# Performance work log

Hardware: AMD Instinct MI355X
Metric: run time of the kernel (lower is better)

Reference implementation:

```python
import jax, jax.numpy as jnp
import numpy as np
from jax import lax

B, N, T, F_IN = 16, 500, 256, 8
H, K, OUT = 64, 3, 1
EPS = 1e-5


def setup_inputs() -> dict:
    key = jax.random.key(0)
    ks = jax.random.split(key, 20)
    def xavier(k, shape):
        fan_in, fan_out = shape[-2], shape[-1]
        lim = np.sqrt(6.0 / (fan_in + fan_out))
        return jax.random.uniform(k, shape, jnp.float32, -lim, lim)
    inp = {
        'x': jax.random.normal(ks[0], (B, N, T, F_IN), jnp.float32),
        'adj': jax.random.uniform(ks[1], (N, N), jnp.float32),
        # temporal conv layer 1: in=F_IN, layer 2: in=H; kernel (1,K), OIHW
        'conv_w1': jax.random.normal(ks[2], (H, F_IN, 1, K), jnp.float32) * 0.1,
        'conv_b1': jnp.zeros((H,), jnp.float32),
        'conv_w2': jax.random.normal(ks[3], (H, H, 1, K), jnp.float32) * 0.05,
        'conv_b2': jnp.zeros((H,), jnp.float32),
        # graph conv weights (in,out) + bias
        'gcn_w1': xavier(ks[4], (H, H)),
        'gcn_b1': jnp.zeros((H,), jnp.float32),
        'gcn_w2': xavier(ks[5], (H, H)),
        'gcn_b2': jnp.zeros((H,), jnp.float32),
        # batchnorm (eval mode: running stats)
        'bn_g1': jnp.ones((H,), jnp.float32),
        'bn_be1': jnp.zeros((H,), jnp.float32),
        'bn_m1': jax.random.normal(ks[6], (H,), jnp.float32) * 0.1,
        'bn_v1': jnp.ones((H,), jnp.float32),
        'bn_g2': jnp.ones((H,), jnp.float32),
        'bn_be2': jnp.zeros((H,), jnp.float32),
        'bn_m2': jax.random.normal(ks[7], (H,), jnp.float32) * 0.1,
        'bn_v2': jnp.ones((H,), jnp.float32),
        # output MLP H -> H//2 -> OUT
        'out_w1': xavier(ks[8], (H, H // 2)),
        'out_bb1': jnp.zeros((H // 2,), jnp.float32),
        'out_w2': xavier(ks[9], (H // 2, OUT)),
        'out_bb2': jnp.zeros((OUT,), jnp.float32),
    }
    return inp


def _layer(x, adj, cw, cb, gw, gb, bg, bb, bm, bv):
    # x: (B, C_in, N, T)
    x = lax.conv_general_dilated(
        x, cw, window_strides=(1, 1), padding=[(0, 0), (K // 2, K // 2)],
        dimension_numbers=('NCHW', 'OIHW', 'NCHW'))
    x = jax.nn.relu(x + cb[None, :, None, None])           # (B,H,N,T)
    # batched graph conv over all timesteps at once
    s = jnp.einsum('bcnt,ch->bhnt', x, gw)                 # support = x @ W
    x = jnp.einsum('mn,bhnt->bhmt', adj, s) + gb[None, :, None, None]
    x = jax.nn.relu(x)
    # batchnorm2d eval over channel dim
    x = (x - bm[None, :, None, None]) * (bg / jnp.sqrt(bv + EPS))[None, :, None, None] + bb[None, :, None, None]
    return x  # dropout is identity in eval


def reference(x, adj, conv_w1, conv_b1, conv_w2, conv_b2,
              gcn_w1, gcn_b1, gcn_w2, gcn_b2,
              bn_g1, bn_be1, bn_m1, bn_v1,
              bn_g2, bn_be2, bn_m2, bn_v2,
              out_w1, out_bb1, out_w2, out_bb2):
    h = jnp.transpose(x, (0, 3, 1, 2))                      # (B,F_in,N,T)
    h = _layer(h, adj, conv_w1, conv_b1, gcn_w1, gcn_b1, bn_g1, bn_be1, bn_m1, bn_v1)
    h = _layer(h, adj, conv_w2, conv_b2, gcn_w2, gcn_b2, bn_g2, bn_be2, bn_m2, bn_v2)
    h = h.mean(axis=-1)                                     # (B,H,N)
    h = jnp.transpose(h, (0, 2, 1))                         # (B,N,H)
    h = jax.nn.relu(h @ out_w1 + out_bb1)
    return h @ out_w2 + out_bb2                             # (B,N,OUT)
```

## Files before the change

### kernel.cpp

```cpp
#include <hip/hip_runtime.h>
#include <hip/hip_bf16.h>


#define BB 16
#define NN 500
#define TT 256
#define FIN 8
#define HH 64

using bf16 = __hip_bfloat16;
typedef __attribute__((ext_vector_type(8))) short short8;
typedef __attribute__((ext_vector_type(4))) short short4v;
typedef __attribute__((ext_vector_type(4))) float f32x4;

static __device__ __forceinline__ short bf16bits(float v) {
    __hip_bfloat16 h = __float2bfloat16(v);
    return *reinterpret_cast<short*>(&h);
}

__global__ __launch_bounds__(256) void k_prep_adj(
    const float* __restrict__ adj, bf16* __restrict__ adjb)
{
    int i = blockIdx.x * 256 + threadIdx.x;
    if (i < 512 * 512) {
        int r = i >> 9, c = i & 511;
        float v = (r < NN && c < NN) ? adj[r * NN + c] : 0.f;
        adjb[i] = __float2bfloat16(v);
    }
}

__global__ __launch_bounds__(256) void k_prep_weights(
    const float* __restrict__ cw1, const float* __restrict__ gw1,
    const float* __restrict__ w2,  const float* __restrict__ gw2,
    bf16* __restrict__ wA1, bf16* __restrict__ gA1,
    bf16* __restrict__ wA2, bf16* __restrict__ gA2)
{
    int i = blockIdx.x * 256 + threadIdx.x;
    if (i < 2048) {
        int h = i >> 5, kp = i & 31, kk = kp >> 3, f = kp & 7;
        wA1[i] = __float2bfloat16(kk < 3 ? cw1[(h * 8 + f) * 3 + kk] : 0.f);
    } else if (i < 6144) {
        int j = i - 2048, h = j >> 6, c = j & 63;
        gA1[j] = __float2bfloat16(gw1[c * 64 + h]);
    } else if (i < 18432) {
        int j = i - 6144, kk = j / 4096, r = j & 4095, co = r >> 6, ci = r & 63;
        wA2[j] = __float2bfloat16(w2[(co * 64 + ci) * 3 + kk]);
    } else if (i < 22528) {
        int j = i - 18432, h = j >> 6, c = j & 63;
        gA2[j] = __float2bfloat16(gw2[c * 64 + h]);
    }
}

__global__ __launch_bounds__(256) void k_conv_mfma1(
    const float* __restrict__ x, const bf16* __restrict__ wA1,
    const bf16* __restrict__ gA1, const float* __restrict__ cb,
    bf16* __restrict__ s_out)
{
    __shared__ __align__(16) short xs[256 * 64];

    const int tid = threadIdx.x;
    const int n = blockIdx.x, lb = blockIdx.y;
    const int lane = tid & 63, w = tid >> 6;
    const int lr = lane & 15, kg = lane >> 4;
    const int t0w = w * 64;

    {
        const float4* gx = (const float4*)(x + (size_t)(lb * NN + n) * (TT * FIN) + tid * 8);
        float4 a = gx[0], b = gx[1];
        short8 v;
        v[0] = bf16bits(a.x); v[1] = bf16bits(a.y); v[2] = bf16bits(a.z); v[3] = bf16bits(a.w);
        v[4] = bf16bits(b.x); v[5] = bf16bits(b.y); v[6] = bf16bits(b.z); v[7] = bf16bits(b.w);
        const int t = tid;
        *(short8*)((char*)xs + t * 128 + (16 ^ ((t & 7) << 4))) = v;
        if (t < 255)
            *(short8*)((char*)xs + (t + 1) * 128 + (0 ^ (((t + 1) & 7) << 4))) = v;
        if (t > 0)
            *(short8*)((char*)xs + (t - 1) * 128 + (32 ^ (((t - 1) & 7) << 4))) = v;
        short8 z = {0, 0, 0, 0, 0, 0, 0, 0};
        *(short8*)((char*)xs + t * 128 + (48 ^ ((t & 7) << 4))) = z;
        if (t == 0)   *(short8*)((char*)xs + 0 * 128 + (0 ^ 0)) = z;
        if (t == 255) *(short8*)((char*)xs + 255 * 128 + (32 ^ ((255 & 7) << 4))) = z;
    }
    __syncthreads();

    f32x4 acc[4][4];
    #pragma unroll
    for (int mi = 0; mi < 4; mi++)
        #pragma unroll
        for (int ti = 0; ti < 4; ti++)
            acc[mi][ti] = (f32x4){0.f, 0.f, 0.f, 0.f};

    const short* wAp = (const short*)wA1;
    {
        short8 af[4], bfr[4];
        #pragma unroll
        for (int mi = 0; mi < 4; mi++)
            af[mi] = *(const short8*)(wAp + (mi * 16 + lr) * 32 + kg * 8);
        #pragma unroll
        for (int ti = 0; ti < 4; ti++) {
            const int row = t0w + ti * 16 + lr;
            bfr[ti] = *(const short8*)((const char*)xs + row * 128 + ((kg * 16) ^ ((row & 7) << 4)));
        }
        #pragma unroll
        for (int ti = 0; ti < 4; ti++)
            #pragma unroll
            for (int mi = 0; mi < 4; mi++)
                acc[mi][ti] = __builtin_amdgcn_mfma_f32_16x16x32_bf16(af[mi], bfr[ti], acc[mi][ti], 0, 0, 0);
    }
    __syncthreads();

    {
        float cbl[16];
        #pragma unroll
        for (int mi = 0; mi < 4; mi++)
            #pragma unroll
            for (int r = 0; r < 4; r++) cbl[mi * 4 + r] = cb[mi * 16 + kg * 4 + r];
        #pragma unroll
        for (int mi = 0; mi < 4; mi++) {
            #pragma unroll
            for (int ti = 0; ti < 4; ti++) {
                const int t = t0w + ti * 16 + lr;
                short4v yv;
                #pragma unroll
                for (int r = 0; r < 4; r++)
                    yv[r] = bf16bits(fmaxf(acc[mi][ti][r] + cbl[mi * 4 + r], 0.f));
                *(short4v*)((char*)xs + t * 128 + ((mi * 32 + kg * 8) ^ ((t & 7) << 4))) = yv;
            }
        }
    }
    __syncthreads();

    f32x4 acc2[4][4];
    #pragma unroll
    for (int mi = 0; mi < 4; mi++)
        #pragma unroll
        for (int ti = 0; ti < 4; ti++)
            acc2[mi][ti] = (f32x4){0.f, 0.f, 0.f, 0.f};

    const short* gAp = (const short*)gA1;
    #pragma unroll
    for (int ks = 0; ks < 2; ks++) {
        short8 af[4], bfr[4];
        #pragma unroll
        for (int mi = 0; mi < 4; mi++)
            af[mi] = *(const short8*)(gAp + (mi * 16 + lr) * 64 + ks * 32 + kg * 8);
        #pragma unroll
        for (int ti = 0; ti < 4; ti++) {
            const int t = t0w + ti * 16 + lr;
            bfr[ti] = *(const short8*)((const char*)xs + t * 128 + ((ks * 64 + kg * 16) ^ ((t & 7) << 4)));
        }
        #pragma unroll
        for (int ti = 0; ti < 4; ti++)
            #pragma unroll
            for (int mi = 0; mi < 4; mi++)
                acc2[mi][ti] = __builtin_amdgcn_mfma_f32_16x16x32_bf16(af[mi], bfr[ti], acc2[mi][ti], 0, 0, 0);
    }

    #pragma unroll
    for (int mi = 0; mi < 4; mi++) {
        #pragma unroll
        for (int r = 0; r < 4; r++) {
            const int h = mi * 16 + kg * 4 + r;
            bf16* orow = s_out + ((size_t)(lb * 64 + h) * NN + n) * TT + t0w + lr;
            #pragma unroll
            for (int ti = 0; ti < 4; ti++)
                orow[ti * 16] = __float2bfloat16(acc2[mi][ti][r]);
        }
    }
}

#define SWZ_T(t) (((((t) & 7) ^ (((t) >> 5) << 1)) & 7) << 4)

template<bool MEAN>
__global__ __launch_bounds__(256) void k_adj_mfma(
    const bf16* __restrict__ s_in, const bf16* __restrict__ adjb,
    const float* __restrict__ gb, const float* __restrict__ bn_g,
    const float* __restrict__ bn_b, const float* __restrict__ bn_m,
    const float* __restrict__ bn_v, bf16* __restrict__ h_out,
    float* __restrict__ pf)
{
    __shared__ __align__(16) short AsS[128 * 72];
    __shared__ __align__(16) short BtS[128 * 64];

    const int tid = threadIdx.x;
    const int m0 = (blockIdx.x >> 1) * 128;
    const int t0 = (blockIdx.x & 1) * 128;
    const int bh = blockIdx.y;
    const int h = bh & 63;

    const int lane = tid & 63;
    const int lr = lane & 15;
    const int kg = lane >> 4;
    const int w = tid >> 6;
    const int wr = w >> 1, wc = w & 1;

    f32x4 acc[4][4];
    #pragma unroll
    for (int mi = 0; mi < 4; mi++)
        #pragma unroll
        for (int ti = 0; ti < 4; ti++)
            acc[mi][ti] = (f32x4){0.f, 0.f, 0.f, 0.f};

    const int ar = tid >> 1, ah = (tid & 1) * 32;
    const int sk = tid >> 2, tseg = (tid & 3) * 32;
    const bf16* sslice = s_in + (size_t)bh * (NN * TT) + t0;

    for (int rnd = 0; rnd < 8; rnd++) {
        const int k0 = rnd * 64;
        {
            const float4* src = (const float4*)(adjb + (size_t)(m0 + ar) * 512 + k0 + ah);
            float4* dst = (float4*)(AsS + ar * 72 + ah);
            dst[0] = src[0]; dst[1] = src[1]; dst[2] = src[2]; dst[3] = src[3];
        }
        {
            const int kglob = k0 + sk;
            short8 v0, v1, v2, v3;
            if (kglob < NN) {
                const short8* g = (const short8*)(sslice + (size_t)kglob * TT + tseg);
                v0 = g[0]; v1 = g[1]; v2 = g[2]; v3 = g[3];
            } else {
                v0 = (short8){0,0,0,0,0,0,0,0}; v1 = v0; v2 = v0; v3 = v0;
            }
            const int kslot = (sk >> 3) << 4;
            const int kfine = (sk & 7) * 2;
            #pragma unroll
            for (int u = 0; u < 4; u++) {
                short8 v = (u == 0) ? v0 : (u == 1) ? v1 : (u == 2) ? v2 : v3;
                #pragma unroll
                for (int j = 0; j < 8; j++) {
                    const int t = tseg + u * 8 + j;
                    *(short*)((char*)BtS + t * 128 + (kslot ^ SWZ_T(t)) + kfine) = v[j];
                }
            }
        }
        __syncthreads();

        #pragma unroll
        for (int ks = 0; ks < 2; ks++) {
            short8 af[4], bfr[4];
            #pragma unroll
            for (int mi = 0; mi < 4; mi++)
                af[mi] = *(const short8*)(AsS + (wr * 64 + mi * 16 + lr) * 72 + ks * 32 + kg * 8);
            #pragma unroll
            for (int ti = 0; ti < 4; ti++) {
                const int t = wc * 64 + ti * 16 + lr;
                bfr[ti] = *(const short8*)((const char*)BtS + t * 128 + ((((ks * 4 + kg) << 4)) ^ SWZ_T(t)));
            }
            #pragma unroll
            for (int ti = 0; ti < 4; ti++)
                #pragma unroll
                for (int mi = 0; mi < 4; mi++)
                    acc[mi][ti] = __builtin_amdgcn_mfma_f32_16x16x32_bf16(af[mi], bfr[ti], acc[mi][ti], 0, 0, 0);
        }
        __syncthreads();
    }

    const float bias  = gb[h];
    const float scale = bn_g[h] / sqrtf(bn_v[h] + 1e-5f);
    const float shift = bn_b[h] - bn_m[h] * scale;

    if constexpr (!MEAN) {
        #pragma unroll
        for (int mi = 0; mi < 4; mi++) {
            const int mbase = m0 + wr * 64 + mi * 16 + kg * 4;
            #pragma unroll
            for (int r = 0; r < 4; r++) {
                const int m = mbase + r;
                if (m < NN) {
                    bf16* orow = h_out + ((size_t)bh * NN + m) * TT + t0 + wc * 64 + lr;
                    #pragma unroll
                    for (int ti = 0; ti < 4; ti++) {
                        float v = fmaxf(acc[mi][ti][r] + bias, 0.f);
                        orow[ti * 16] = __float2bfloat16(v * scale + shift);
                    }
                }
            }
        }
    } else {
        float sums[4][4];
        #pragma unroll
        for (int mi = 0; mi < 4; mi++)
            #pragma unroll
            for (int r = 0; r < 4; r++) {
                float s = 0.f;
                #pragma unroll
                for (int ti = 0; ti < 4; ti++)
                    s += fmaxf(acc[mi][ti][r] + bias, 0.f) * scale + shift;
                sums[mi][r] = s;
            }
        #pragma unroll
        for (int off = 1; off < 16; off <<= 1)
            #pragma unroll
            for (int mi = 0; mi < 4; mi++)
                #pragma unroll
                for (int r = 0; r < 4; r++)
                    sums[mi][r] += __shfl_xor(sums[mi][r], off, 64);
        if (lr == 0) {
            const size_t stride = (size_t)gridDim.y * NN;
            float* pfb = pf + ((size_t)((blockIdx.x & 1) * 2 + wc)) * stride + (size_t)bh * NN;
            #pragma unroll
            for (int mi = 0; mi < 4; mi++) {
                const int m = m0 + wr * 64 + mi * 16 + kg * 4;
                if (m < NN) {
                    float4 v = make_float4(sums[mi][0], sums[mi][1], sums[mi][2], sums[mi][3]);
                    *(float4*)(pfb + m) = v;
                }
            }
        }
    }
}

__global__ __launch_bounds__(256) void k_conv_mfma2(
    const bf16* __restrict__ hin, const bf16* __restrict__ wA,
    const bf16* __restrict__ gA, const float* __restrict__ cb,
    bf16* __restrict__ s_out)
{
    __shared__ __align__(16) short xs[258 * 64];

    const int tid = threadIdx.x;
    const int n = blockIdx.x, lb = blockIdx.y;
    const int lane = tid & 63, w = tid >> 6;
    const int lr = lane & 15, kg = lane >> 4;
    const int t0w = w * 64;

    const bf16* base = hin + ((size_t)lb * 64 * NN + n) * TT;

    {
        const int cin = tid >> 2, tq = (tid & 3) * 64;
        const short* gsrc = (const short*)(base + (size_t)cin * (NN * TT) + tq);
        #pragma unroll
        for (int i = 0; i < 8; i++) {
            short8 v = *(const short8*)(gsrc + i * 8);
            #pragma unroll
            for (int j = 0; j < 8; j++) {
                const int row = tq + i * 8 + j + 1;
                const int addr = row * 128 + ((cin * 2) ^ ((row & 7) << 4));
                *(short*)((char*)xs + addr) = v[j];
            }
        }
        if (tid < 64) {
            *(short*)((char*)xs + (tid * 2)) = 0;
            *(short*)((char*)xs + 257 * 128 + ((tid * 2) ^ 16)) = 0;
        }
    }
    __syncthreads();

    f32x4 acc[4][4];
    #pragma unroll
    for (int mi = 0; mi < 4; mi++)
        #pragma unroll
        for (int ti = 0; ti < 4; ti++)
            acc[mi][ti] = (f32x4){0.f, 0.f, 0.f, 0.f};

    const short* wAp = (const short*)wA;
    #pragma unroll
    for (int kk = 0; kk < 3; kk++) {
        #pragma unroll
        for (int ks = 0; ks < 2; ks++) {
            short8 af[4], bfr[4];
            #pragma unroll
            for (int mi = 0; mi < 4; mi++)
                af[mi] = *(const short8*)(wAp + ((kk * 64 + mi * 16 + lr) * 64 + ks * 32 + kg * 8));
            #pragma unroll
            for (int ti = 0; ti < 4; ti++) {
                const int row = t0w + ti * 16 + lr + kk;
                const int addr = row * 128 + ((ks * 64 + kg * 16) ^ ((row & 7) << 4));
                bfr[ti] = *(const short8*)((const char*)xs + addr);
            }
            #pragma unroll
            for (int ti = 0; ti < 4; ti++)
                #pragma unroll
                for (int mi = 0; mi < 4; mi++)
                    acc[mi][ti] = __builtin_amdgcn_mfma_f32_16x16x32_bf16(af[mi], bfr[ti], acc[mi][ti], 0, 0, 0);
        }
    }
    __syncthreads();

    {
        float cbl[16];
        #pragma unroll
        for (int mi = 0; mi < 4; mi++)
            #pragma unroll
            for (int r = 0; r < 4; r++) cbl[mi * 4 + r] = cb[mi * 16 + kg * 4 + r];
        #pragma unroll
        for (int mi = 0; mi < 4; mi++) {
            #pragma unroll
            for (int ti = 0; ti < 4; ti++) {
                const int t = t0w + ti * 16 + lr;
                short4v yv;
                #pragma unroll
                for (int r = 0; r < 4; r++)
                    yv[r] = bf16bits(fmaxf(acc[mi][ti][r] + cbl[mi * 4 + r], 0.f));
                const int addr = t * 128 + ((mi * 32 + kg * 8) ^ ((t & 7) << 4));
                *(short4v*)((char*)xs + addr) = yv;
            }
        }
    }
    __syncthreads();

    f32x4 acc2[4][4];
    #pragma unroll
    for (int mi = 0; mi < 4; mi++)
        #pragma unroll
        for (int ti = 0; ti < 4; ti++)
            acc2[mi][ti] = (f32x4){0.f, 0.f, 0.f, 0.f};

    const short* gAp = (const short*)gA;
    #pragma unroll
    for (int ks = 0; ks < 2; ks++) {
        short8 af[4], bfr[4];
        #pragma unroll
        for (int mi = 0; mi < 4; mi++)
            af[mi] = *(const short8*)(gAp + ((mi * 16 + lr) * 64 + ks * 32 + kg * 8));
        #pragma unroll
        for (int ti = 0; ti < 4; ti++) {
            const int t = t0w + ti * 16 + lr;
            const int addr = t * 128 + ((ks * 64 + kg * 16) ^ ((t & 7) << 4));
            bfr[ti] = *(const short8*)((const char*)xs + addr);
        }
        #pragma unroll
        for (int ti = 0; ti < 4; ti++)
            #pragma unroll
            for (int mi = 0; mi < 4; mi++)
                acc2[mi][ti] = __builtin_amdgcn_mfma_f32_16x16x32_bf16(af[mi], bfr[ti], acc2[mi][ti], 0, 0, 0);
    }

    #pragma unroll
    for (int mi = 0; mi < 4; mi++) {
        #pragma unroll
        for (int r = 0; r < 4; r++) {
            const int h = mi * 16 + kg * 4 + r;
            bf16* orow = s_out + ((size_t)(lb * 64 + h) * NN + n) * TT + t0w + lr;
            #pragma unroll
            for (int ti = 0; ti < 4; ti++)
                orow[ti * 16] = __float2bfloat16(acc2[mi][ti][r]);
        }
    }
}

__global__ __launch_bounds__(64) void k_mlp(
    const float* __restrict__ pf, int nbh,
    const float* __restrict__ w1, const float* __restrict__ b1,
    const float* __restrict__ w2, const float* __restrict__ b2,
    float* __restrict__ out)
{
    __shared__ float mm[64];
    __shared__ float hid[32];
    const int n = blockIdx.x, lb = blockIdx.y, tid = threadIdx.x;

    const size_t stride = (size_t)nbh * NN;
    const size_t idx = (size_t)(lb * 64 + tid) * NN + n;
    float s = pf[idx] + pf[stride + idx] + pf[2 * stride + idx] + pf[3 * stride + idx];
    mm[tid] = s * (1.f / 256.f);
    __syncthreads();
    if (tid < 32) {
        float a = b1[tid];
        #pragma unroll
        for (int c = 0; c < 64; c++) a += mm[c] * w1[c * 32 + tid];
        hid[tid] = fmaxf(a, 0.f);
    }
    __syncthreads();
    if (tid == 0) {
        float a = b2[0];
        #pragma unroll
        for (int j = 0; j < 32; j++) a += hid[j] * w2[j];
        out[lb * NN + n] = a;
    }
}

extern "C" void kernel_launch(void* const* d_in, const int* in_sizes, int n_in,
                              void* d_out, int out_size, void* d_ws, size_t ws_size,
                              hipStream_t stream) {
    const float* x       = (const float*)d_in[0];
    const float* adj     = (const float*)d_in[1];
    const float* conv_w1 = (const float*)d_in[2];
    const float* conv_b1 = (const float*)d_in[3];
    const float* conv_w2 = (const float*)d_in[4];
    const float* conv_b2 = (const float*)d_in[5];
    const float* gcn_w1  = (const float*)d_in[6];
    const float* gcn_b1  = (const float*)d_in[7];
    const float* gcn_w2  = (const float*)d_in[8];
    const float* gcn_b2  = (const float*)d_in[9];
    const float* bn_g1   = (const float*)d_in[10];
    const float* bn_be1  = (const float*)d_in[11];
    const float* bn_m1   = (const float*)d_in[12];
    const float* bn_v1   = (const float*)d_in[13];
    const float* bn_g2   = (const float*)d_in[14];
    const float* bn_be2  = (const float*)d_in[15];
    const float* bn_m2   = (const float*)d_in[16];
    const float* bn_v2   = (const float*)d_in[17];
    const float* out_w1  = (const float*)d_in[18];
    const float* out_b1  = (const float*)d_in[19];
    const float* out_w2  = (const float*)d_in[20];
    const float* out_b2  = (const float*)d_in[21];
    float* out = (float*)d_out;

    const size_t per_b = (size_t)HH * NN * TT;
    const size_t reserve = 1 << 20;
    const size_t bytes_per_b_both = per_b * 2 * 2;
    int chunk = (int)((ws_size > reserve ? ws_size - reserve : 0) / bytes_per_b_both);
    if (chunk > BB) chunk = BB;
    if (chunk < 1) chunk = 1;

    char* ws = (char*)d_ws;
    bf16* adjb = (bf16*)ws;
    bf16* wA2  = (bf16*)(ws + 0x80000);
    bf16* gA2  = (bf16*)(ws + 0x80000 + 24576);
    bf16* wA1  = (bf16*)(ws + 0x80000 + 32768);
    bf16* gA1  = (bf16*)(ws + 0x80000 + 36864);
    bf16* bufA = (bf16*)(ws + reserve);
    bf16* bufB = bufA + (size_t)chunk * per_b;

    k_prep_adj<<<1024, 256, 0, stream>>>(adj, adjb);
    k_prep_weights<<<88, 256, 0, stream>>>(conv_w1, gcn_w1, conv_w2, gcn_w2,
                                           wA1, gA1, wA2, gA2);

    for (int b0 = 0; b0 < BB; b0 += chunk) {
        const int nb = (BB - b0) < chunk ? (BB - b0) : chunk;
        float* pf = (float*)bufB;

        k_conv_mfma1<<<dim3(NN, nb), 256, 0, stream>>>(
            x + (size_t)b0 * NN * TT * FIN, wA1, gA1, conv_b1, bufA);

        k_adj_mfma<false><<<dim3(8, nb * 64), 256, 0, stream>>>(
            bufA, adjb, gcn_b1, bn_g1, bn_be1, bn_m1, bn_v1, bufB, nullptr);

        k_conv_mfma2<<<dim3(NN, nb), 256, 0, stream>>>(
            bufB, wA2, gA2, conv_b2, bufA);

        k_adj_mfma<true><<<dim3(8, nb * 64), 256, 0, stream>>>(
            bufA, adjb, gcn_b2, bn_g2, bn_be2, bn_m2, bn_v2, nullptr, pf);

        k_mlp<<<dim3(NN, nb), 64, 0, stream>>>(
            pf, nb * 64, out_w1, out_b1, out_w2, out_b2, out + (size_t)b0 * NN);
    }
}
```

Before: 744.1 us.

## Remap adjacency GEMM blocks per XCD and read adj fragments directly from global

Flattens the adjacency-GEMM grid to one dimension and remaps block IDs so that all four m-tiles of one (batch,channel,t-half) slice run on the same XCD, improving L2 reuse of the s slice. Drops the LDS staging of the adjacency A tile; each wave now loads its bf16 adj fragments straight from global memory, relying on cache hits for the small shared 512x512 matrix. The B-tile transpose into LDS now writes 4-element vectors instead of single shorts, cutting LDS store count. This trades LDS traffic for more global/L2 loads on the A operand.

```diff
diff --git a/kernel.cpp b/kernel.cpp
--- a/kernel.cpp
+++ b/kernel.cpp
@@ -177,15 +177,19 @@
     const float* __restrict__ gb, const float* __restrict__ bn_g,
     const float* __restrict__ bn_b, const float* __restrict__ bn_m,
     const float* __restrict__ bn_v, bf16* __restrict__ h_out,
-    float* __restrict__ pf)
+    float* __restrict__ pf, int nbh)
 {
-    __shared__ __align__(16) short AsS[128 * 72];
     __shared__ __align__(16) short BtS[128 * 64];
 
     const int tid = threadIdx.x;
-    const int m0 = (blockIdx.x >> 1) * 128;
-    const int t0 = (blockIdx.x & 1) * 128;
-    const int bh = blockIdx.y;
+    const int id = blockIdx.x;
+    const int xcd = id & 7;
+    const int jj = id >> 3;
+    const int mt = jj & 3;
+    const int g = ((jj >> 2) << 3) + xcd;
+    const int bh = g >> 1;
+    const int m0 = mt * 128;
+    const int t0 = (g & 1) * 128;
     const int h = bh & 63;
 
     const int lane = tid & 63;
@@ -201,36 +205,27 @@
         for (int ti = 0; ti < 4; ti++)
             acc[mi][ti] = (f32x4){0.f, 0.f, 0.f, 0.f};
 
-    const int ar = tid >> 1, ah = (tid & 1) * 32;
-    const int sk = tid >> 2, tseg = (tid & 3) * 32;
-    const bf16* sslice = s_in + (size_t)bh * (NN * TT) + t0;
+    const int q = tid >> 4;
+    const int tg = tid & 15;
+    const bf16* sslice = s_in + (size_t)bh * (NN * TT) + t0 + tg * 8;
+    const short* adjp = (const short*)adjb;
 
     for (int rnd = 0; rnd < 8; rnd++) {
         const int k0 = rnd * 64;
         {
-            const float4* src = (const float4*)(adjb + (size_t)(m0 + ar) * 512 + k0 + ah);
-            float4* dst = (float4*)(AsS + ar * 72 + ah);
-            dst[0] = src[0]; dst[1] = src[1]; dst[2] = src[2]; dst[3] = src[3];
-        }
-        {
-            const int kglob = k0 + sk;
-            short8 v0, v1, v2, v3;
-            if (kglob < NN) {
-                const short8* g = (const short8*)(sslice + (size_t)kglob * TT + tseg);
-                v0 = g[0]; v1 = g[1]; v2 = g[2]; v3 = g[3];
-            } else {
-                v0 = (short8){0,0,0,0,0,0,0,0}; v1 = v0; v2 = v0; v3 = v0;
-            }
-            const int kslot = (sk >> 3) << 4;
-            const int kfine = (sk & 7) * 2;
-            #pragma unroll
-            for (int u = 0; u < 4; u++) {
-                short8 v = (u == 0) ? v0 : (u == 1) ? v1 : (u == 2) ? v2 : v3;
-                #pragma unroll
-                for (int j = 0; j < 8; j++) {
-                    const int t = tseg + u * 8 + j;
-                    *(short*)((char*)BtS + t * 128 + (kslot ^ SWZ_T(t)) + kfine) = v[j];
-                }
+            short8 vq[4];
+            #pragma unroll
+            for (int kq = 0; kq < 4; kq++) {
+                const int kglob = k0 + q * 4 + kq;
+                vq[kq] = (kglob < NN) ? *(const short8*)(sslice + (size_t)kglob * TT)
+                                      : (short8){0, 0, 0, 0, 0, 0, 0, 0};
+            }
+            #pragma unroll
+            for (int jW = 0; jW < 8; jW++) {
+                const int t = tg * 8 + jW;
+                short4v wv;
+                wv[0] = vq[0][jW]; wv[1] = vq[1][jW]; wv[2] = vq[2][jW]; wv[3] = vq[3][jW];
+                *(short4v*)((char*)BtS + t * 128 + ((((q >> 1) << 4)) ^ SWZ_T(t)) + (q & 1) * 8) = wv;
             }
         }
         __syncthreads();
@@ -240,7 +235,8 @@
             short8 af[4], bfr[4];
             #pragma unroll
             for (int mi = 0; mi < 4; mi++)
-                af[mi] = *(const short8*)(AsS + (wr * 64 + mi * 16 + lr) * 72 + ks * 32 + kg * 8);
+                af[mi] = *(const short8*)(adjp +
+                    (size_t)(m0 + wr * 64 + mi * 16 + lr) * 512 + k0 + ks * 32 + kg * 8);
             #pragma unroll
             for (int ti = 0; ti < 4; ti++) {
                 const int t = wc * 64 + ti * 16 + lr;
@@ -296,8 +292,8 @@
                 for (int r = 0; r < 4; r++)
                     sums[mi][r] += __shfl_xor(sums[mi][r], off, 64);
         if (lr == 0) {
-            const size_t stride = (size_t)gridDim.y * NN;
-            float* pfb = pf + ((size_t)((blockIdx.x & 1) * 2 + wc)) * stride + (size_t)bh * NN;
+            const size_t stride = (size_t)nbh * NN;
+            float* pfb = pf + ((size_t)((g & 1) * 2 + wc)) * stride + (size_t)bh * NN;
             #pragma unroll
             for (int mi = 0; mi < 4; mi++) {
                 const int m = m0 + wr * 64 + mi * 16 + kg * 4;
@@ -517,21 +513,22 @@
 
     for (int b0 = 0; b0 < BB; b0 += chunk) {
         const int nb = (BB - b0) < chunk ? (BB - b0) : chunk;
+        const int nbh = nb * 64;
         float* pf = (float*)bufB;
 
         k_conv_mfma1<<<dim3(NN, nb), 256, 0, stream>>>(
             x + (size_t)b0 * NN * TT * FIN, wA1, gA1, conv_b1, bufA);
 
-        k_adj_mfma<false><<<dim3(8, nb * 64), 256, 0, stream>>>(
-            bufA, adjb, gcn_b1, bn_g1, bn_be1, bn_m1, bn_v1, bufB, nullptr);
+        k_adj_mfma<false><<<dim3(8 * nbh), 256, 0, stream>>>(
+            bufA, adjb, gcn_b1, bn_g1, bn_be1, bn_m1, bn_v1, bufB, nullptr, nbh);
 
         k_conv_mfma2<<<dim3(NN, nb), 256, 0, stream>>>(
             bufB, wA2, gA2, conv_b2, bufA);
 
-        k_adj_mfma<true><<<dim3(8, nb * 64), 256, 0, stream>>>(
-            bufA, adjb, gcn_b2, bn_g2, bn_be2, bn_m2, bn_v2, nullptr, pf);
+        k_adj_mfma<true><<<dim3(8 * nbh), 256, 0, stream>>>(
+            bufA, adjb, gcn_b2, bn_g2, bn_be2, bn_m2, bn_v2, nullptr, pf, nbh);
 
         k_mlp<<<dim3(NN, nb), 64, 0, stream>>>(
-            pf, nb * 64, out_w1, out_b1, out_w2, out_b2, out + (size_t)b0 * NN);
-    }
-}
+            pf, nbh, out_w1, out_b1, out_w2, out_b2, out + (size_t)b0 * NN);
+    }
+}
```

Result: slower. 918.2 us (+23.4%).
